# Kernel optimization log

Measured on AMD Instinct MI355X. Metric: run time of the kernel, lower is better.

Reference implementation:

```python
import jax, jax.numpy as jnp
import numpy as np
from jax import lax

B, C, O, H, W = 32, 128, 256, 56, 56
BN_EPS = 1e-5
DW_THR = 4.0     # cut_conv2_3_DW threshold
PW_THR = 1e-3    # cut_conv2_3_PW threshold


def setup_inputs() -> dict:
    key = jax.random.key(0)
    ks = jax.random.split(key, 8)
    x = jax.random.normal(ks[0], (B, C, H, W), jnp.float32)
    # depthwise conv params: groups=C -> weight [C,1,3,3]
    dw_w = jax.random.normal(ks[1], (C, 1, 3, 3), jnp.float32) * 0.3
    dw_b = jax.random.normal(ks[2], (C,), jnp.float32) * 0.1
    dw_gamma = jnp.ones((C,), jnp.float32) + 0.1 * jax.random.normal(ks[3], (C,), jnp.float32)
    dw_beta = 0.1 * jax.random.normal(ks[4], (C,), jnp.float32)
    dw_mean = jnp.zeros((C,), jnp.float32)
    dw_var = jnp.ones((C,), jnp.float32)
    # pointwise 1x1 conv: weight [O,C,1,1] -> stored as [O,C]
    pw_w = jax.random.normal(ks[5], (O, C), jnp.float32) * 0.05
    pw_b = jax.random.normal(ks[6], (O,), jnp.float32) * 0.1
    pw_gamma = jnp.ones((O,), jnp.float32) + 0.1 * jax.random.normal(ks[7], (O,), jnp.float32)
    pw_beta = jnp.zeros((O,), jnp.float32)
    pw_mean = jnp.zeros((O,), jnp.float32)
    pw_var = jnp.ones((O,), jnp.float32)
    return {"x": x, "dw_w": dw_w, "dw_b": dw_b, "dw_gamma": dw_gamma,
            "dw_beta": dw_beta, "dw_mean": dw_mean, "dw_var": dw_var,
            "pw_w": pw_w, "pw_b": pw_b, "pw_gamma": pw_gamma,
            "pw_beta": pw_beta, "pw_mean": pw_mean, "pw_var": pw_var}


def _bn(x, gamma, beta, mean, var):
    scale = (gamma * lax.rsqrt(var + BN_EPS))[None, :, None, None]
    shift = (beta - mean * gamma * lax.rsqrt(var + BN_EPS))[None, :, None, None]
    return x * scale + shift


def _channel_cut(x, thr):
    # zero the full HxW plane of any (sample, channel) whose abs-max < thr
    maxabs = jnp.max(jnp.abs(x), axis=(2, 3), keepdims=True)  # [B,C',1,1]
    return jnp.where(maxabs < thr, jnp.zeros_like(x), x)


def reference(x, dw_w, dw_b, dw_gamma, dw_beta, dw_mean, dw_var,
              pw_w, pw_b, pw_gamma, pw_beta, pw_mean, pw_var):
    # depthwise 3x3 conv, padding=1, groups=C
    y = lax.conv_general_dilated(
        x, dw_w, window_strides=(1, 1), padding=((1, 1), (1, 1)),
        dimension_numbers=("NCHW", "OIHW", "NCHW"), feature_group_count=C)
    y = y + dw_b[None, :, None, None]
    y = jax.nn.relu(_bn(y, dw_gamma, dw_beta, dw_mean, dw_var))
    y = _channel_cut(y, DW_THR)
    # pointwise 1x1 conv == channel-mixing GEMM
    z = jnp.einsum("bchw,oc->bohw", y, pw_w) + pw_b[None, :, None, None]
    z = jax.nn.relu(_bn(z, pw_gamma, pw_beta, pw_mean, pw_var))
    z = _channel_cut(z, PW_THR)
    return z
```

## Files before the change

kernel.cpp:

```cpp
#include <hip/hip_runtime.h>
#include <math.h>

#define BB 32
#define CC 128
#define OO 256
#define HWSZ 3136
#define HW4 (HWSZ*4)
#define BN_EPS 1e-5f
#define DW_THR 4.0f

typedef __attribute__((ext_vector_type(8))) short short8;
typedef __attribute__((ext_vector_type(4))) float f32x4;
typedef __attribute__((ext_vector_type(4))) unsigned uint4v;
typedef __attribute__((ext_vector_type(2))) unsigned uint2v;

__device__ __forceinline__ unsigned bf16rne(float v) {
    unsigned u = __builtin_bit_cast(unsigned, v);
    return (u + 0x7fffu + ((u >> 16) & 1u)) >> 16;
}
__device__ __forceinline__ unsigned pack2(float a, float b) {
    return bf16rne(a) | (bf16rne(b) << 16);
}

__global__ __launch_bounds__(256) void prep_kernel(
    const float* __restrict__ pw_w, const float* __restrict__ pw_b,
    const float* __restrict__ pw_gamma, const float* __restrict__ pw_beta,
    const float* __restrict__ pw_mean, const float* __restrict__ pw_var,
    unsigned short* __restrict__ wb, float* __restrict__ bias2)
{
    const int idx = blockIdx.x * 256 + threadIdx.x;
    const int o = idx >> 7;
    const float s = pw_gamma[o] * rsqrtf(pw_var[o] + BN_EPS);
    wb[idx] = (unsigned short)bf16rne(pw_w[idx] * s);
    if (idx < OO) {
        const float s2 = pw_gamma[idx] * rsqrtf(pw_var[idx] + BN_EPS);
        bias2[idx] = pw_b[idx] * s2 + pw_beta[idx] - pw_mean[idx] * s2;
    }
}

__global__ __launch_bounds__(256) void dw_kernel(
    const float* __restrict__ x, const float* __restrict__ dw_w,
    const float* __restrict__ dw_b, const float* __restrict__ dw_gamma,
    const float* __restrict__ dw_beta, const float* __restrict__ dw_mean,
    const float* __restrict__ dw_var, unsigned short* __restrict__ y,
    uint2v* __restrict__ mask64)
{
    const int cg = blockIdx.x;
    const int b  = blockIdx.y;
    const int tid = threadIdx.x;
    const int c0 = cg * 4;

    float wk[4][9], sc[4], bi[4];
#pragma unroll
    for (int c = 0; c < 4; ++c) {
        const int ch = c0 + c;
#pragma unroll
        for (int j = 0; j < 9; ++j) wk[c][j] = dw_w[ch * 9 + j];
        const float s = dw_gamma[ch] * rsqrtf(dw_var[ch] + BN_EPS);
        sc[c] = s;
        bi[c] = dw_b[ch] * s + dw_beta[ch] - dw_mean[ch] * s;
    }

    float cmax[4] = {0.f, 0.f, 0.f, 0.f};
    unsigned short* yp = y + ((size_t)(b * 32 + cg)) * HW4;

#pragma unroll
    for (int is = 0; is < 4; ++is) {
        const int s = tid + is * 256;
        if (s < 784) {
            const int r  = s / 14;
            const int m  = s - r * 14;
            const int q4 = m * 4;
            float vals[4][4];
#pragma unroll
            for (int c = 0; c < 4; ++c) {
                const float* px = x + ((size_t)(b * CC + c0 + c)) * HWSZ;
                float a0 = 0.f, a1 = 0.f, a2 = 0.f, a3 = 0.f;
#pragma unroll
                for (int dr = 0; dr < 3; ++dr) {
                    const int rr = r + dr - 1;
                    const bool vr2 = (rr >= 0) && (rr < 56);
                    const float* prow = px + rr * 56 + q4;
                    float4 M = vr2 ? *(const float4*)prow
                                   : make_float4(0.f, 0.f, 0.f, 0.f);
                    float xm = (vr2 && m > 0)  ? prow[-1] : 0.f;
                    float xp = (vr2 && m < 13) ? prow[4]  : 0.f;
                    const float w0 = wk[c][dr*3+0];
                    const float w1 = wk[c][dr*3+1];
                    const float w2 = wk[c][dr*3+2];
                    a0 += w0*xm  + w1*M.x + w2*M.y;
                    a1 += w0*M.x + w1*M.y + w2*M.z;
                    a2 += w0*M.y + w1*M.z + w2*M.w;
                    a3 += w0*M.z + w1*M.w + w2*xp;
                }
                float v0 = fmaxf(a0*sc[c]+bi[c], 0.f);
                float v1 = fmaxf(a1*sc[c]+bi[c], 0.f);
                float v2 = fmaxf(a2*sc[c]+bi[c], 0.f);
                float v3 = fmaxf(a3*sc[c]+bi[c], 0.f);
                vals[c][0] = v0; vals[c][1] = v1;
                vals[c][2] = v2; vals[c][3] = v3;
                cmax[c] = fmaxf(cmax[c], fmaxf(fmaxf(v0, v1), fmaxf(v2, v3)));
            }
            uint4 p0, p1;
            p0.x = pack2(vals[0][0], vals[1][0]);
            p0.y = pack2(vals[2][0], vals[3][0]);
            p0.z = pack2(vals[0][1], vals[1][1]);
            p0.w = pack2(vals[2][1], vals[3][1]);
            p1.x = pack2(vals[0][2], vals[1][2]);
            p1.y = pack2(vals[2][2], vals[3][2]);
            p1.z = pack2(vals[0][3], vals[1][3]);
            p1.w = pack2(vals[2][3], vals[3][3]);
            *(uint4*)(yp + (size_t)s * 16)     = p0;
            *(uint4*)(yp + (size_t)s * 16 + 8) = p1;
        }
    }

#pragma unroll
    for (int c = 0; c < 4; ++c)
#pragma unroll
        for (int off = 32; off; off >>= 1)
            cmax[c] = fmaxf(cmax[c], __shfl_xor(cmax[c], off, 64));
    __shared__ float smax[4][4];
    if ((tid & 63) == 0) {
#pragma unroll
        for (int c = 0; c < 4; ++c) smax[tid >> 6][c] = cmax[c];
    }
    __syncthreads();
    if (tid == 0) {
        unsigned mw[4];
#pragma unroll
        for (int c = 0; c < 4; ++c) {
            float mx = fmaxf(fmaxf(smax[0][c], smax[1][c]),
                             fmaxf(smax[2][c], smax[3][c]));
            mw[c] = (mx < DW_THR) ? 0u : 0xFFFFu;
        }
        uint2v mv;
        mv.x = mw[0] | (mw[1] << 16);
        mv.y = mw[2] | (mw[3] << 16);
        mask64[b * 32 + cg] = mv;
    }
}

__global__ __launch_bounds__(256) void pw_kernel(
    const unsigned short* __restrict__ yt,
    const unsigned short* __restrict__ wb,
    const float* __restrict__ bias2,
    const uint2v* __restrict__ mask64,
    float* __restrict__ out)
{
    const int n0 = blockIdx.x * 64;
    const int b  = blockIdx.y;
    const int tid = threadIdx.x;
    const int ow  = (tid >> 6) * 64;
    const int l   = tid & 63;
    const int g   = l >> 4;
    const int lan = l & 15;

    const unsigned short* yb = yt + (size_t)b * (32 * HW4);

    uint4v mk[4];
    const uint2v* mb = mask64 + b * 32;
#pragma unroll
    for (int kk = 0; kk < 4; ++kk)
        mk[kk] = *(const uint4v*)&mb[kk * 8 + 2 * g];

    float bv[4];
#pragma unroll
    for (int orr = 0; orr < 4; ++orr)
        bv[orr] = bias2[ow + orr * 16 + lan];

    f32x4 acc[4][4] = {};

#pragma unroll
    for (int kk = 0; kk < 4; ++kk) {
        short8 bfr[4];
#pragma unroll
        for (int orr = 0; orr < 4; ++orr)
            bfr[orr] = *(const short8*)(wb
                + (size_t)(ow + orr * 16 + lan) * CC + kk * 32 + g * 8);
#pragma unroll
        for (int mr = 0; mr < 4; ++mr) {
            const unsigned short* ya = yb + (size_t)(kk * 8 + 2 * g) * HW4
                                       + (size_t)(n0 + mr * 16 + lan) * 4;
            uint2v lo = *(const uint2v*)ya;
            uint2v hi = *(const uint2v*)(ya + HW4);
            uint4v w4;
            w4.x = lo.x & mk[kk].x;
            w4.y = lo.y & mk[kk].y;
            w4.z = hi.x & mk[kk].z;
            w4.w = hi.y & mk[kk].w;
            const short8 a = __builtin_bit_cast(short8, w4);
#pragma unroll
            for (int orr = 0; orr < 4; ++orr)
                acc[mr][orr] = __builtin_amdgcn_mfma_f32_16x16x32_bf16(
                    a, bfr[orr], acc[mr][orr], 0, 0, 0);
        }
    }

#pragma unroll
    for (int mr = 0; mr < 4; ++mr) {
#pragma unroll
        for (int orr = 0; orr < 4; ++orr) {
            const int o = ow + orr * 16 + lan;
            float4 r;
            r.x = fmaxf(acc[mr][orr][0] + bv[orr], 0.f);
            r.y = fmaxf(acc[mr][orr][1] + bv[orr], 0.f);
            r.z = fmaxf(acc[mr][orr][2] + bv[orr], 0.f);
            r.w = fmaxf(acc[mr][orr][3] + bv[orr], 0.f);
            *(float4*)&out[((size_t)b * OO + o) * HWSZ
                           + n0 + mr * 16 + g * 4] = r;
        }
    }
}

extern "C" void kernel_launch(void* const* d_in, const int* in_sizes, int n_in,
                              void* d_out, int out_size, void* d_ws, size_t ws_size,
                              hipStream_t stream)
{
    const float* x        = (const float*)d_in[0];
    const float* dw_w     = (const float*)d_in[1];
    const float* dw_b     = (const float*)d_in[2];
    const float* dw_gamma = (const float*)d_in[3];
    const float* dw_beta  = (const float*)d_in[4];
    const float* dw_mean  = (const float*)d_in[5];
    const float* dw_var   = (const float*)d_in[6];
    const float* pw_w     = (const float*)d_in[7];
    const float* pw_b     = (const float*)d_in[8];
    const float* pw_gamma = (const float*)d_in[9];
    const float* pw_beta  = (const float*)d_in[10];
    const float* pw_mean  = (const float*)d_in[11];
    const float* pw_var   = (const float*)d_in[12];

    unsigned short* yws  = (unsigned short*)d_ws;
    unsigned short* wbuf = (unsigned short*)((char*)d_ws + 25690112);
    float*          b2   = (float*)((char*)d_ws + 25690112 + 65536);
    uint2v*         msk  = (uint2v*)((char*)d_ws + 25690112 + 65536 + 1024);

    prep_kernel<<<128, 256, 0, stream>>>(pw_w, pw_b, pw_gamma, pw_beta,
                                         pw_mean, pw_var, wbuf, b2);

    dim3 g1(32, 32);
    dw_kernel<<<g1, 256, 0, stream>>>(x, dw_w, dw_b, dw_gamma, dw_beta,
                                      dw_mean, dw_var, yws, msk);

    dim3 g2(49, 32);
    pw_kernel<<<g2, 256, 0, stream>>>(yws, wbuf, b2, msk, (float*)d_out);
}
```

Baseline: 204.3 us.

## Interleave 8 channels in intermediate layout and prepack weights into MFMA fragments

The depthwise kernel now processes 8 channels per block and stores the bf16 intermediate interleaved by 8 channels, so the pointwise kernel loads each MFMA A fragment with a single 16-byte load instead of two 8-byte loads. The prep kernel writes pointwise weights pre-arranged in MFMA fragment order so B loads are contiguous per lane. Output stores become nontemporal to avoid cache pollution. The trade-off is fewer depthwise blocks (512 instead of 1024), higher register pressure from 8 channels, and a non-unrolled outer loop.

```diff
diff --git a/kernel.cpp b/kernel.cpp
--- a/kernel.cpp
+++ b/kernel.cpp
@@ -5,14 +5,13 @@
 #define CC 128
 #define OO 256
 #define HWSZ 3136
-#define HW4 (HWSZ*4)
+#define HW8 (HWSZ*8)
 #define BN_EPS 1e-5f
 #define DW_THR 4.0f
 
 typedef __attribute__((ext_vector_type(8))) short short8;
 typedef __attribute__((ext_vector_type(4))) float f32x4;
 typedef __attribute__((ext_vector_type(4))) unsigned uint4v;
-typedef __attribute__((ext_vector_type(2))) unsigned uint2v;
 
 __device__ __forceinline__ unsigned bf16rne(float v) {
     unsigned u = __builtin_bit_cast(unsigned, v);
@@ -26,15 +25,28 @@
     const float* __restrict__ pw_w, const float* __restrict__ pw_b,
     const float* __restrict__ pw_gamma, const float* __restrict__ pw_beta,
     const float* __restrict__ pw_mean, const float* __restrict__ pw_var,
-    unsigned short* __restrict__ wb, float* __restrict__ bias2)
-{
-    const int idx = blockIdx.x * 256 + threadIdx.x;
-    const int o = idx >> 7;
+    unsigned short* __restrict__ wfrag, float* __restrict__ bias2)
+{
+    const int t = blockIdx.x * 256 + threadIdx.x;
+    const int w   = t >> 10;
+    const int kk  = (t >> 8) & 3;
+    const int orr = (t >> 6) & 3;
+    const int l   = t & 63;
+    const int g   = l >> 4, lan = l & 15;
+    const int o   = w * 64 + orr * 16 + lan;
     const float s = pw_gamma[o] * rsqrtf(pw_var[o] + BN_EPS);
-    wb[idx] = (unsigned short)bf16rne(pw_w[idx] * s);
-    if (idx < OO) {
-        const float s2 = pw_gamma[idx] * rsqrtf(pw_var[idx] + BN_EPS);
-        bias2[idx] = pw_b[idx] * s2 + pw_beta[idx] - pw_mean[idx] * s2;
+    const float* src = pw_w + (size_t)o * CC + kk * 32 + g * 8;
+    const float4 A = *(const float4*)src;
+    const float4 Bv = *(const float4*)(src + 4);
+    uint4 pk;
+    pk.x = pack2(A.x * s, A.y * s);
+    pk.y = pack2(A.z * s, A.w * s);
+    pk.z = pack2(Bv.x * s, Bv.y * s);
+    pk.w = pack2(Bv.z * s, Bv.w * s);
+    *(uint4*)(wfrag + (size_t)t * 8) = pk;
+    if (t < OO) {
+        const float s2 = pw_gamma[t] * rsqrtf(pw_var[t] + BN_EPS);
+        bias2[t] = pw_b[t] * s2 + pw_beta[t] - pw_mean[t] * s2;
     }
 }
 
@@ -43,16 +55,16 @@
     const float* __restrict__ dw_b, const float* __restrict__ dw_gamma,
     const float* __restrict__ dw_beta, const float* __restrict__ dw_mean,
     const float* __restrict__ dw_var, unsigned short* __restrict__ y,
-    uint2v* __restrict__ mask64)
+    uint4v* __restrict__ mask8)
 {
     const int cg = blockIdx.x;
     const int b  = blockIdx.y;
     const int tid = threadIdx.x;
-    const int c0 = cg * 4;
-
-    float wk[4][9], sc[4], bi[4];
-#pragma unroll
-    for (int c = 0; c < 4; ++c) {
+    const int c0 = cg * 8;
+
+    float wk[8][9], sc[8], bi[8];
+#pragma unroll
+    for (int c = 0; c < 8; ++c) {
         const int ch = c0 + c;
 #pragma unroll
         for (int j = 0; j < 9; ++j) wk[c][j] = dw_w[ch * 9 + j];
@@ -61,19 +73,19 @@
         bi[c] = dw_b[ch] * s + dw_beta[ch] - dw_mean[ch] * s;
     }
 
-    float cmax[4] = {0.f, 0.f, 0.f, 0.f};
-    unsigned short* yp = y + ((size_t)(b * 32 + cg)) * HW4;
-
-#pragma unroll
+    float cmax[8] = {};
+    unsigned short* yp = y + ((size_t)(b * 16 + cg)) * HW8;
+
+#pragma unroll 1
     for (int is = 0; is < 4; ++is) {
         const int s = tid + is * 256;
         if (s < 784) {
             const int r  = s / 14;
             const int m  = s - r * 14;
             const int q4 = m * 4;
-            float vals[4][4];
-#pragma unroll
-            for (int c = 0; c < 4; ++c) {
+            float vals[8][4];
+#pragma unroll
+            for (int c = 0; c < 8; ++c) {
                 const float* px = x + ((size_t)(b * CC + c0 + c)) * HWSZ;
                 float a0 = 0.f, a1 = 0.f, a2 = 0.f, a3 = 0.f;
 #pragma unroll
@@ -93,81 +105,80 @@
                     a2 += w0*M.y + w1*M.z + w2*M.w;
                     a3 += w0*M.z + w1*M.w + w2*xp;
                 }
-                float v0 = fmaxf(a0*sc[c]+bi[c], 0.f);
-                float v1 = fmaxf(a1*sc[c]+bi[c], 0.f);
-                float v2 = fmaxf(a2*sc[c]+bi[c], 0.f);
-                float v3 = fmaxf(a3*sc[c]+bi[c], 0.f);
-                vals[c][0] = v0; vals[c][1] = v1;
-                vals[c][2] = v2; vals[c][3] = v3;
-                cmax[c] = fmaxf(cmax[c], fmaxf(fmaxf(v0, v1), fmaxf(v2, v3)));
+                vals[c][0] = fmaxf(a0*sc[c]+bi[c], 0.f);
+                vals[c][1] = fmaxf(a1*sc[c]+bi[c], 0.f);
+                vals[c][2] = fmaxf(a2*sc[c]+bi[c], 0.f);
+                vals[c][3] = fmaxf(a3*sc[c]+bi[c], 0.f);
+                cmax[c] = fmaxf(cmax[c],
+                    fmaxf(fmaxf(vals[c][0], vals[c][1]),
+                          fmaxf(vals[c][2], vals[c][3])));
             }
-            uint4 p0, p1;
-            p0.x = pack2(vals[0][0], vals[1][0]);
-            p0.y = pack2(vals[2][0], vals[3][0]);
-            p0.z = pack2(vals[0][1], vals[1][1]);
-            p0.w = pack2(vals[2][1], vals[3][1]);
-            p1.x = pack2(vals[0][2], vals[1][2]);
-            p1.y = pack2(vals[2][2], vals[3][2]);
-            p1.z = pack2(vals[0][3], vals[1][3]);
-            p1.w = pack2(vals[2][3], vals[3][3]);
-            *(uint4*)(yp + (size_t)s * 16)     = p0;
-            *(uint4*)(yp + (size_t)s * 16 + 8) = p1;
-        }
-    }
-
-#pragma unroll
-    for (int c = 0; c < 4; ++c)
+#pragma unroll
+            for (int p = 0; p < 4; ++p) {
+                uint4 pk;
+                pk.x = pack2(vals[0][p], vals[1][p]);
+                pk.y = pack2(vals[2][p], vals[3][p]);
+                pk.z = pack2(vals[4][p], vals[5][p]);
+                pk.w = pack2(vals[6][p], vals[7][p]);
+                *(uint4*)(yp + (size_t)(s * 4 + p) * 8) = pk;
+            }
+        }
+    }
+
+#pragma unroll
+    for (int c = 0; c < 8; ++c)
 #pragma unroll
         for (int off = 32; off; off >>= 1)
             cmax[c] = fmaxf(cmax[c], __shfl_xor(cmax[c], off, 64));
-    __shared__ float smax[4][4];
+    __shared__ float smax[4][8];
     if ((tid & 63) == 0) {
 #pragma unroll
-        for (int c = 0; c < 4; ++c) smax[tid >> 6][c] = cmax[c];
+        for (int c = 0; c < 8; ++c) smax[tid >> 6][c] = cmax[c];
     }
     __syncthreads();
     if (tid == 0) {
-        unsigned mw[4];
-#pragma unroll
-        for (int c = 0; c < 4; ++c) {
+        unsigned mw[8];
+#pragma unroll
+        for (int c = 0; c < 8; ++c) {
             float mx = fmaxf(fmaxf(smax[0][c], smax[1][c]),
                              fmaxf(smax[2][c], smax[3][c]));
             mw[c] = (mx < DW_THR) ? 0u : 0xFFFFu;
         }
-        uint2v mv;
+        uint4v mv;
         mv.x = mw[0] | (mw[1] << 16);
         mv.y = mw[2] | (mw[3] << 16);
-        mask64[b * 32 + cg] = mv;
+        mv.z = mw[4] | (mw[5] << 16);
+        mv.w = mw[6] | (mw[7] << 16);
+        mask8[b * 16 + cg] = mv;
     }
 }
 
 __global__ __launch_bounds__(256) void pw_kernel(
     const unsigned short* __restrict__ yt,
-    const unsigned short* __restrict__ wb,
+    const unsigned short* __restrict__ wfrag,
     const float* __restrict__ bias2,
-    const uint2v* __restrict__ mask64,
+    const uint4v* __restrict__ mask8,
     float* __restrict__ out)
 {
     const int n0 = blockIdx.x * 64;
     const int b  = blockIdx.y;
     const int tid = threadIdx.x;
-    const int ow  = (tid >> 6) * 64;
+    const int w   = tid >> 6;
     const int l   = tid & 63;
     const int g   = l >> 4;
     const int lan = l & 15;
 
-    const unsigned short* yb = yt + (size_t)b * (32 * HW4);
+    const unsigned short* yb = yt + (size_t)b * (16 * HW8);
 
     uint4v mk[4];
-    const uint2v* mb = mask64 + b * 32;
 #pragma unroll
     for (int kk = 0; kk < 4; ++kk)
-        mk[kk] = *(const uint4v*)&mb[kk * 8 + 2 * g];
+        mk[kk] = mask8[b * 16 + kk * 4 + g];
 
     float bv[4];
 #pragma unroll
     for (int orr = 0; orr < 4; ++orr)
-        bv[orr] = bias2[ow + orr * 16 + lan];
+        bv[orr] = bias2[w * 64 + orr * 16 + lan];
 
     f32x4 acc[4][4] = {};
 
@@ -176,20 +187,14 @@
         short8 bfr[4];
 #pragma unroll
         for (int orr = 0; orr < 4; ++orr)
-            bfr[orr] = *(const short8*)(wb
-                + (size_t)(ow + orr * 16 + lan) * CC + kk * 32 + g * 8);
+            bfr[orr] = *(const short8*)(wfrag
+                + ((size_t)((w * 4 + kk) * 4 + orr) * 64 + l) * 8);
 #pragma unroll
         for (int mr = 0; mr < 4; ++mr) {
-            const unsigned short* ya = yb + (size_t)(kk * 8 + 2 * g) * HW4
-                                       + (size_t)(n0 + mr * 16 + lan) * 4;
-            uint2v lo = *(const uint2v*)ya;
-            uint2v hi = *(const uint2v*)(ya + HW4);
-            uint4v w4;
-            w4.x = lo.x & mk[kk].x;
-            w4.y = lo.y & mk[kk].y;
-            w4.z = hi.x & mk[kk].z;
-            w4.w = hi.y & mk[kk].w;
-            const short8 a = __builtin_bit_cast(short8, w4);
+            uint4v a4 = *(const uint4v*)(yb + (size_t)(kk * 4 + g) * HW8
+                                         + (size_t)(n0 + mr * 16 + lan) * 8);
+            a4 &= mk[kk];
+            const short8 a = __builtin_bit_cast(short8, a4);
 #pragma unroll
             for (int orr = 0; orr < 4; ++orr)
                 acc[mr][orr] = __builtin_amdgcn_mfma_f32_16x16x32_bf16(
@@ -201,14 +206,15 @@
     for (int mr = 0; mr < 4; ++mr) {
 #pragma unroll
         for (int orr = 0; orr < 4; ++orr) {
-            const int o = ow + orr * 16 + lan;
-            float4 r;
+            const int o = w * 64 + orr * 16 + lan;
+            f32x4 r;
             r.x = fmaxf(acc[mr][orr][0] + bv[orr], 0.f);
             r.y = fmaxf(acc[mr][orr][1] + bv[orr], 0.f);
             r.z = fmaxf(acc[mr][orr][2] + bv[orr], 0.f);
             r.w = fmaxf(acc[mr][orr][3] + bv[orr], 0.f);
-            *(float4*)&out[((size_t)b * OO + o) * HWSZ
-                           + n0 + mr * 16 + g * 4] = r;
+            __builtin_nontemporal_store(r,
+                (f32x4*)&out[((size_t)b * OO + o) * HWSZ
+                             + n0 + mr * 16 + g * 4]);
         }
     }
 }
@@ -234,12 +240,12 @@
     unsigned short* yws  = (unsigned short*)d_ws;
     unsigned short* wbuf = (unsigned short*)((char*)d_ws + 25690112);
     float*          b2   = (float*)((char*)d_ws + 25690112 + 65536);
-    uint2v*         msk  = (uint2v*)((char*)d_ws + 25690112 + 65536 + 1024);
-
-    prep_kernel<<<128, 256, 0, stream>>>(pw_w, pw_b, pw_gamma, pw_beta,
-                                         pw_mean, pw_var, wbuf, b2);
-
-    dim3 g1(32, 32);
+    uint4v*         msk  = (uint4v*)((char*)d_ws + 25690112 + 65536 + 1024);
+
+    prep_kernel<<<16, 256, 0, stream>>>(pw_w, pw_b, pw_gamma, pw_beta,
+                                        pw_mean, pw_var, wbuf, b2);
+
+    dim3 g1(16, 32);
     dw_kernel<<<g1, 256, 0, stream>>>(x, dw_w, dw_b, dw_gamma, dw_beta,
                                       dw_mean, dw_var, yws, msk);
 
```

Measured after the change: 204.6 us. About the same (+0.1%).
